# Kernel optimization log

Measured on AMD Instinct MI355X. Metric: run time of the kernel, lower is better.

Reference implementation:

```python
import jax, jax.numpy as jnp
import numpy as np

EMBED_DIM = 768
NUM_HEADS = 12
HEAD_DIM = EMBED_DIM // NUM_HEADS
B, N = 16, 512


def setup_inputs() -> dict:
    key = jax.random.key(0)
    ks = jax.random.split(key, 13)
    s = 1.0 / np.sqrt(EMBED_DIM)
    return {
        "query": jax.random.normal(ks[0], (B, N, EMBED_DIM), jnp.float32),
        "key_in": jax.random.normal(ks[1], (B, N, EMBED_DIM), jnp.float32),
        "value": jax.random.normal(ks[2], (B, N, EMBED_DIM), jnp.float32),
        "spatial_bias": jax.random.normal(ks[3], (B, N, N), jnp.float32),
        "edge_bias": jax.random.normal(ks[4], (B, N, N), jnp.float32),
        "Wq": jax.random.uniform(ks[5], (EMBED_DIM, EMBED_DIM), jnp.float32, -s, s),
        "bq": jax.random.uniform(ks[6], (EMBED_DIM,), jnp.float32, -s, s),
        "Wk": jax.random.uniform(ks[7], (EMBED_DIM, EMBED_DIM), jnp.float32, -s, s),
        "bk": jax.random.uniform(ks[8], (EMBED_DIM,), jnp.float32, -s, s),
        "Wv": jax.random.uniform(ks[9], (EMBED_DIM, EMBED_DIM), jnp.float32, -s, s),
        "bv": jax.random.uniform(ks[10], (EMBED_DIM,), jnp.float32, -s, s),
        "Wo": jax.random.uniform(ks[11], (EMBED_DIM, EMBED_DIM), jnp.float32, -s, s),
        "bo": jax.random.uniform(ks[12], (EMBED_DIM,), jnp.float32, -s, s),
    }


def reference(query, key_in, value, spatial_bias, edge_bias,
              Wq, bq, Wk, bk, Wv, bv, Wo, bo):
    b, n, e = query.shape
    h, d = NUM_HEADS, HEAD_DIM
    scale = d ** -0.5
    # projections (torch Linear: x @ W.T + b), reshape to [b, h, n, d]
    Q = (query @ Wq.T + bq).reshape(b, n, h, d).transpose(0, 2, 1, 3)
    K = (key_in @ Wk.T + bk).reshape(b, n, h, d).transpose(0, 2, 1, 3)
    V = (value @ Wv.T + bv).reshape(b, n, h, d).transpose(0, 2, 1, 3)
    # scores: [b, h, n, n] with additive spatial + edge bias broadcast over heads
    scores = jnp.einsum('bhnd,bhmd->bhnm', Q, K) * scale
    scores = scores + spatial_bias[:, None, :, :] + edge_bias[:, None, :, :]
    attn_weights = jax.nn.softmax(scores, axis=-1)
    attn_output = jnp.einsum('bhnm,bhmd->bhnd', attn_weights, V)
    attn_output = attn_output.transpose(0, 2, 1, 3).reshape(b, n, e)
    attn_output = attn_output @ Wo.T + bo
    return attn_output, attn_weights
```

## Files before the change

kernel.cpp:

```cpp
#include <hip/hip_runtime.h>

using bf16x8 = __attribute__((ext_vector_type(8))) __bf16;
using f32x4  = __attribute__((ext_vector_type(4))) float;
using u16 = unsigned short;

constexpr int Bb = 16, Nn = 512, Ee = 768, Hh = 12, Dd = 64;

__device__ inline u16 f2b(float x) {
  union { float f; unsigned int u; } v; v.f = x;
  unsigned int r = v.u + 0x7fffu + ((v.u >> 16) & 1u);
  return (u16)(r >> 16);
}

__device__ inline unsigned cvtpk(float lo, float hi) {
  unsigned r;
  asm("v_cvt_pk_bf16_f32 %0, %1, %2" : "=v"(r) : "v"(lo), "v"(hi));
  return r;
}

__device__ inline void gload16(const void* g, void* l) {
  __builtin_amdgcn_global_load_lds((const __attribute__((address_space(1))) void*)g,
                                   (__attribute__((address_space(3))) void*)l, 16, 0, 0);
}

#define MFMA __builtin_amdgcn_mfma_f32_16x16x32_bf16

__global__ void k_cvtw(const float* __restrict__ w0, const float* __restrict__ w1,
                       const float* __restrict__ w2, const float* __restrict__ w3,
                       u16* __restrict__ dst) {
  int idx = blockIdx.x * 256 + threadIdx.x;
  constexpr int per = Ee * Ee / 4;
  int m = idx / per, r = idx - m * per;
  const float* src = (m == 0) ? w0 : (m == 1) ? w1 : (m == 2) ? w2 : w3;
  float4 v = reinterpret_cast<const float4*>(src)[r];
  ushort4 o = make_ushort4(f2b(v.x), f2b(v.y), f2b(v.z), f2b(v.w));
  reinterpret_cast<ushort4*>(dst)[idx] = o;
}

__global__ void k_biascomb(const float* __restrict__ sb, const float* __restrict__ eb,
                           u16* __restrict__ cb) {
  int idx = blockIdx.x * 256 + threadIdx.x;
  float4 s0 = reinterpret_cast<const float4*>(sb)[idx * 2];
  float4 s1 = reinterpret_cast<const float4*>(sb)[idx * 2 + 1];
  float4 e0 = reinterpret_cast<const float4*>(eb)[idx * 2];
  float4 e1 = reinterpret_cast<const float4*>(eb)[idx * 2 + 1];
  ushort4 o0 = make_ushort4(f2b(s0.x + e0.x), f2b(s0.y + e0.y), f2b(s0.z + e0.z), f2b(s0.w + e0.w));
  ushort4 o1 = make_ushort4(f2b(s1.x + e1.x), f2b(s1.y + e1.y), f2b(s1.z + e1.z), f2b(s1.w + e1.w));
  reinterpret_cast<ushort4*>(cb)[idx * 2] = o0;
  reinterpret_cast<ushort4*>(cb)[idx * 2 + 1] = o1;
}

__global__ __launch_bounds__(256, 3)
void k_qkv(const float* __restrict__ xq, const float* __restrict__ xk, const float* __restrict__ xv,
           const u16* __restrict__ wb, const float* __restrict__ bq, const float* __restrict__ bk,
           const float* __restrict__ bv, u16* __restrict__ Q, u16* __restrict__ K,
           u16* __restrict__ VT) {
  const int mat = blockIdx.z;
  const float* X = (mat == 0) ? xq : (mat == 1) ? xk : xv;
  const u16* W = wb + (size_t)mat * Ee * Ee;
  const float* bias = (mat == 0) ? bq : (mat == 1) ? bk : bv;
  const int bm = blockIdx.x, bn = blockIdx.y;
  const int tid = threadIdx.x, lane = tid & 63, wid = tid >> 6;
  const int wr = wid >> 1, wc = wid & 1;

  __shared__ char smem[49152];

  auto stageA = [&](int buf, int it) {
    const int r0 = tid >> 3, s = tid & 7;
    char* lbase = smem + buf * 16384 + tid * 16;
#pragma unroll
    for (int R = 0; R < 4; ++R) {
      const int row = R * 32 + r0;
      const int ch = s ^ (row & 7);
      gload16(X + (size_t)(bm * 128 + row) * Ee + it * 32 + ch * 4, lbase + R * 4096);
    }
  };
  auto stageB = [&](int buf, int it) {
    const int r0 = tid >> 2, s = tid & 3;
    char* lbase = smem + 32768 + buf * 8192 + tid * 16;
#pragma unroll
    for (int R = 0; R < 2; ++R) {
      const int row = R * 64 + r0;
      const int ch = s ^ ((row >> 1) & 3);
      gload16(W + (size_t)(bn * 128 + row) * Ee + it * 32 + ch * 8, lbase + R * 4096);
    }
  };

  f32x4 acc[4][4] = {};

  auto compute = [&](int buf) {
    const char* Ab = smem + buf * 16384;
    const char* Bbp = smem + 32768 + buf * 8192;
    const int q = lane >> 4;
    bf16x8 a[4], b[4];
#pragma unroll
    for (int mt = 0; mt < 4; ++mt) {
      const int row = wr * 64 + mt * 16 + (lane & 15);
      const int s0 = (2 * q) ^ (row & 7), s1 = (2 * q + 1) ^ (row & 7);
      f32x4 f0 = *reinterpret_cast<const f32x4*>(Ab + row * 128 + s0 * 16);
      f32x4 f1 = *reinterpret_cast<const f32x4*>(Ab + row * 128 + s1 * 16);
      union { unsigned u[4]; bf16x8 v; } cv;
      cv.u[0] = cvtpk(f0[0], f0[1]);
      cv.u[1] = cvtpk(f0[2], f0[3]);
      cv.u[2] = cvtpk(f1[0], f1[1]);
      cv.u[3] = cvtpk(f1[2], f1[3]);
      a[mt] = cv.v;
    }
#pragma unroll
    for (int nt = 0; nt < 4; ++nt) {
      const int row = wc * 64 + nt * 16 + (lane & 15);
      const int s = q ^ ((row >> 1) & 3);
      b[nt] = *reinterpret_cast<const bf16x8*>(Bbp + row * 64 + s * 16);
    }
#pragma unroll
    for (int mt = 0; mt < 4; ++mt)
#pragma unroll
      for (int nt = 0; nt < 4; ++nt)
        acc[mt][nt] = MFMA(a[mt], b[nt], acc[mt][nt], 0, 0, 0);
  };

  stageA(0, 0); stageB(0, 0);
  __syncthreads();
  int buf = 0;
  for (int it = 0; it < 24; ++it) {
    if (it + 1 < 24) { stageA(buf ^ 1, it + 1); stageB(buf ^ 1, it + 1); }
    compute(buf);
    __syncthreads();
    buf ^= 1;
  }

  u16* sm16 = (u16*)smem;
  if (mat < 2) {
    u16* dst = (mat == 0) ? Q : K;
    const float sc = (mat == 0) ? 0.125f : 1.0f;
#pragma unroll
    for (int mt = 0; mt < 4; ++mt) {
      const int n_l0 = wr * 64 + mt * 16 + ((lane >> 4) << 2);
#pragma unroll
      for (int nt = 0; nt < 4; ++nt) {
        const int e_l = wc * 64 + nt * 16 + (lane & 15);
        const float bs = bias[bn * 128 + e_l];
#pragma unroll
        for (int j = 0; j < 4; ++j)
          sm16[(n_l0 + j) * 136 + e_l] = f2b((acc[mt][nt][j] + bs) * sc);
      }
    }
    __syncthreads();
    const int row = tid >> 1, half = tid & 1;
    const int n = bm * 128 + row, b = n >> 9, n0 = n & 511, h = bn * 2 + half;
    u16* gp = dst + ((size_t)(b * Hh + h) * Nn + n0) * Dd;
    const u16* sp = sm16 + row * 136 + half * 64;
#pragma unroll
    for (int i = 0; i < 8; ++i)
      *reinterpret_cast<int4*>(gp + i * 8) = *reinterpret_cast<const int4*>(sp + i * 8);
  } else {
#pragma unroll
    for (int mt = 0; mt < 4; ++mt) {
      const int n_l0 = wr * 64 + mt * 16 + ((lane >> 4) << 2);
#pragma unroll
      for (int nt = 0; nt < 4; ++nt) {
        const int e_l = wc * 64 + nt * 16 + (lane & 15);
        const float bs = bias[bn * 128 + e_l];
#pragma unroll
        for (int j = 0; j < 4; ++j)
          sm16[e_l * 136 + n_l0 + j] = f2b(acc[mt][nt][j] + bs);
      }
    }
    __syncthreads();
    const int er = tid >> 1, half = tid & 1;
    const int b = bm >> 2, h = bn * 2 + (er >> 6), d = er & 63;
    u16* gp = VT + ((size_t)(b * Hh + h) * Dd + d) * Nn + (bm & 3) * 128 + half * 64;
    const u16* sp = sm16 + er * 136 + half * 64;
#pragma unroll
    for (int i = 0; i < 8; ++i)
      *reinterpret_cast<int4*>(gp + i * 8) = *reinterpret_cast<const int4*>(sp + i * 8);
  }
}

__global__ __launch_bounds__(256, 2)
void k_attn(const u16* __restrict__ Q, const u16* __restrict__ K,
            const u16* __restrict__ cb, const u16* __restrict__ VT,
            float* __restrict__ wout, u16* __restrict__ AO) {
  const int qb = blockIdx.x, h = blockIdx.y, b = blockIdx.z;
  const int bh = b * Hh + h;
  const int q0 = qb * 64;
  const int tid = threadIdx.x, lane = tid & 63, wid = tid >> 6;
  const int l15 = lane & 15, q4 = lane >> 4;

  __shared__ char smem[65536];

  bf16x8 aq[2];
  {
    const u16* qp = Q + ((size_t)bh * Nn + q0 + wid * 16 + l15) * Dd + q4 * 8;
    aq[0] = *reinterpret_cast<const bf16x8*>(qp);
    aq[1] = *reinterpret_cast<const bf16x8*>(qp + 32);
  }

#pragma unroll
  for (int i = 0; i < 16; ++i) {
    const int s = i * 256 + tid;
    const int row = s >> 3, cs = s & 7;
    gload16(K + ((size_t)bh * Nn + row) * Dd + (cs ^ (row & 7)) * 8, smem + s * 16);
  }
  __syncthreads();

  f32x4 acc[32] = {};
#pragma unroll
  for (int kt = 0; kt < 8; ++kt)
#pragma unroll
    for (int kk = 0; kk < 2; ++kk)
#pragma unroll
      for (int ct = 0; ct < 4; ++ct) {
        const int r = kt * 64 + ct * 16 + l15;
        bf16x8 bk = *reinterpret_cast<const bf16x8*>(
            smem + r * 128 + (((kk * 4 + q4) ^ (r & 7)) * 16));
        acc[kt * 4 + ct] = MFMA(bk, aq[kk], acc[kt * 4 + ct], 0, 0, 0);
      }

  const int rql = wid * 16 + l15;
  const int rq = q0 + rql;
  const u16* cbp = cb + ((size_t)b * Nn + rq) * Nn + q4 * 4;
  uint2 cbr[32];
#pragma unroll
  for (int t = 0; t < 32; ++t)
    cbr[t] = *reinterpret_cast<const uint2*>(cbp + t * 16);
#pragma unroll
  for (int t = 0; t < 32; ++t) {
    acc[t][0] += __uint_as_float((unsigned)cbr[t].x << 16);
    acc[t][1] += __uint_as_float(cbr[t].x & 0xffff0000u);
    acc[t][2] += __uint_as_float((unsigned)cbr[t].y << 16);
    acc[t][3] += __uint_as_float(cbr[t].y & 0xffff0000u);
  }

  float mx = -1e30f;
#pragma unroll
  for (int t = 0; t < 32; ++t)
#pragma unroll
    for (int j = 0; j < 4; ++j) mx = fmaxf(mx, acc[t][j]);
  mx = fmaxf(mx, __shfl_xor(mx, 16));
  mx = fmaxf(mx, __shfl_xor(mx, 32));

  float sum = 0.f;
#pragma unroll
  for (int t = 0; t < 32; ++t)
#pragma unroll
    for (int j = 0; j < 4; ++j) {
      float p = exp2f((acc[t][j] - mx) * 1.44269504f);
      acc[t][j] = p;
      sum += p;
    }
  sum += __shfl_xor(sum, 16);
  sum += __shfl_xor(sum, 32);
  const float inv = 1.0f / sum;

  __syncthreads();

  const u16* Vb = VT + ((size_t)bh * Dd + l15) * Nn + q4 * 8;
  bf16x8 vb0[8], vb1[8];
  auto loadV = [&](int kt, bf16x8* d) {
#pragma unroll
    for (int kk = 0; kk < 2; ++kk)
#pragma unroll
      for (int ct = 0; ct < 4; ++ct)
        d[kk * 4 + ct] = *reinterpret_cast<const bf16x8*>(
            Vb + (size_t)(ct * 16) * Nn + kt * 64 + kk * 32);
  };
  loadV(0, vb0);
  loadV(1, vb1);

  f32x4* wp4 = reinterpret_cast<f32x4*>(wout + ((size_t)bh * Nn + rq) * Nn);
  char* Pb = smem + rql * 1024;
#pragma unroll
  for (int t = 0; t < 32; ++t) {
    f32x4 o;
    o[0] = acc[t][0] * inv; o[1] = acc[t][1] * inv;
    o[2] = acc[t][2] * inv; o[3] = acc[t][3] * inv;
    __builtin_nontemporal_store(o, &wp4[t * 4 + q4]);
    uint2 pk;
    pk.x = cvtpk(o[0], o[1]);
    pk.y = cvtpk(o[2], o[3]);
    const int chunk = (2 * t + (q4 >> 1)) ^ (rql & 7);
    *reinterpret_cast<uint2*>(Pb + chunk * 16 + (q4 & 1) * 8) = pk;
  }
  __syncthreads();

  f32x4 acc2[4] = {};
  const int qr = rql;
  const char* Pr = smem + qr * 1024;
#pragma unroll
  for (int kp = 0; kp < 4; ++kp) {
    const int ktA = 2 * kp, ktB = 2 * kp + 1;
#pragma unroll
    for (int kk = 0; kk < 2; ++kk) {
      const int chunk = (ktA * 8 + kk * 4 + q4) ^ (qr & 7);
      bf16x8 pa = *reinterpret_cast<const bf16x8*>(Pr + chunk * 16);
#pragma unroll
      for (int ct = 0; ct < 4; ++ct)
        acc2[ct] = MFMA(pa, vb0[kk * 4 + ct], acc2[ct], 0, 0, 0);
    }
    if (ktA + 2 < 8) loadV(ktA + 2, vb0);
#pragma unroll
    for (int kk = 0; kk < 2; ++kk) {
      const int chunk = (ktB * 8 + kk * 4 + q4) ^ (qr & 7);
      bf16x8 pa = *reinterpret_cast<const bf16x8*>(Pr + chunk * 16);
#pragma unroll
      for (int ct = 0; ct < 4; ++ct)
        acc2[ct] = MFMA(pa, vb1[kk * 4 + ct], acc2[ct], 0, 0, 0);
    }
    if (ktB + 2 < 8) loadV(ktB + 2, vb1);
  }

  __syncthreads();
  u16* ao_t = (u16*)smem;
#pragma unroll
  for (int ct = 0; ct < 4; ++ct)
#pragma unroll
    for (int j = 0; j < 4; ++j)
      ao_t[(wid * 16 + q4 * 4 + j) * 72 + ct * 16 + l15] = f2b(acc2[ct][j]);
  __syncthreads();
  {
    const int row = tid >> 3, ch = tid & 7;
#pragma unroll
    for (int i = 0; i < 2; ++i) {
      const int r = row + i * 32;
      int4 v = *reinterpret_cast<const int4*>(ao_t + r * 72 + ch * 8);
      *reinterpret_cast<int4*>(AO + ((size_t)b * Nn + q0 + r) * Ee + h * Dd + ch * 8) = v;
    }
  }
}

__global__ __launch_bounds__(256, 4)
void k_outproj(const u16* __restrict__ AOp, const u16* __restrict__ Wo,
               const float* __restrict__ bo, float* __restrict__ out) {
  const int bm = blockIdx.x, bn = blockIdx.y;
  const int tid = threadIdx.x, lane = tid & 63, wid = tid >> 6;
  const int wr = wid >> 1, wc = wid & 1;

  __shared__ char smem[32768];

  auto stage = [&](const u16* src, int lds_base, int buf, int it) {
    const int r0 = tid >> 2, s = tid & 3;
    char* lbase = smem + lds_base + buf * 8192 + tid * 16;
#pragma unroll
    for (int R = 0; R < 2; ++R) {
      const int row = R * 64 + r0;
      const int ch = s ^ ((row >> 1) & 3);
      gload16(src + (size_t)row * Ee + it * 32 + ch * 8, lbase + R * 4096);
    }
  };

  f32x4 acc[4][4] = {};

  auto compute = [&](int buf) {
    const char* Ab = smem + buf * 8192;
    const char* Bbp = smem + 16384 + buf * 8192;
    const int q = lane >> 4;
    bf16x8 a[4], b[4];
#pragma unroll
    for (int mt = 0; mt < 4; ++mt) {
      const int row = wr * 64 + mt * 16 + (lane & 15);
      const int s = q ^ ((row >> 1) & 3);
      a[mt] = *reinterpret_cast<const bf16x8*>(Ab + row * 64 + s * 16);
    }
#pragma unroll
    for (int nt = 0; nt < 4; ++nt) {
      const int row = wc * 64 + nt * 16 + (lane & 15);
      const int s = q ^ ((row >> 1) & 3);
      b[nt] = *reinterpret_cast<const bf16x8*>(Bbp + row * 64 + s * 16);
    }
#pragma unroll
    for (int mt = 0; mt < 4; ++mt)
#pragma unroll
      for (int nt = 0; nt < 4; ++nt)
        acc[mt][nt] = MFMA(a[mt], b[nt], acc[mt][nt], 0, 0, 0);
  };

  const u16* Asrc = AOp + (size_t)(bm * 128) * Ee;
  const u16* Bsrc = Wo + (size_t)(bn * 128) * Ee;
  stage(Asrc, 0, 0, 0); stage(Bsrc, 16384, 0, 0);
  __syncthreads();
  int buf = 0;
  for (int it = 0; it < 24; ++it) {
    if (it + 1 < 24) { stage(Asrc, 0, buf ^ 1, it + 1); stage(Bsrc, 16384, buf ^ 1, it + 1); }
    compute(buf);
    __syncthreads();
    buf ^= 1;
  }

#pragma unroll
  for (int mt = 0; mt < 4; ++mt) {
#pragma unroll
    for (int nt = 0; nt < 4; ++nt) {
      const int ecol = bn * 128 + wc * 64 + nt * 16 + (lane & 15);
      const int r0 = bm * 128 + wr * 64 + mt * 16 + ((lane >> 4) << 2);
      const float bs = bo[ecol];
      f32x4 v = acc[mt][nt];
#pragma unroll
      for (int j = 0; j < 4; ++j)
        out[(size_t)(r0 + j) * Ee + ecol] = v[j] + bs;
    }
  }
}

extern "C" void kernel_launch(void* const* d_in, const int* in_sizes, int n_in,
                              void* d_out, int out_size, void* d_ws, size_t ws_size,
                              hipStream_t stream) {
  const float* query  = (const float*)d_in[0];
  const float* key_in = (const float*)d_in[1];
  const float* value  = (const float*)d_in[2];
  const float* sb     = (const float*)d_in[3];
  const float* eb     = (const float*)d_in[4];
  const float* Wq     = (const float*)d_in[5];
  const float* bq     = (const float*)d_in[6];
  const float* Wk     = (const float*)d_in[7];
  const float* bk     = (const float*)d_in[8];
  const float* Wv     = (const float*)d_in[9];
  const float* bv     = (const float*)d_in[10];
  const float* Wo     = (const float*)d_in[11];
  const float* bo     = (const float*)d_in[12];

  float* out0 = (float*)d_out;
  float* wout = out0 + (size_t)Bb * Nn * Ee;

  char* ws = (char*)d_ws;
  const size_t off_wb = 0;
  const size_t off_Q  = 4718592;
  const size_t off_K  = 17301504;
  const size_t off_VT = 29884416;
  const size_t off_AO = 42467328;
  const size_t off_cb = 55050240;
  if (ws_size < 63438848) return;

  u16* wb  = (u16*)(ws + off_wb);
  u16* Qs  = (u16*)(ws + off_Q);
  u16* Kst = (u16*)(ws + off_K);
  u16* VTs = (u16*)(ws + off_VT);
  u16* AO  = (u16*)(ws + off_AO);
  u16* cbf = (u16*)(ws + off_cb);

  k_cvtw<<<2304, 256, 0, stream>>>(Wq, Wk, Wv, Wo, wb);
  k_biascomb<<<2048, 256, 0, stream>>>(sb, eb, cbf);
  k_qkv<<<dim3(64, 6, 3), 256, 0, stream>>>(query, key_in, value, wb, bq, bk, bv, Qs, Kst, VTs);
  k_attn<<<dim3(8, Hh, Bb), 256, 0, stream>>>(Qs, Kst, cbf, VTs, wout, AO);
  k_outproj<<<dim3(64, 6), 256, 0, stream>>>(AO, wb + 3 * Ee * Ee, bo, out0);
}
```

Before: 196.3 us.

## Fuse conversion kernels, remap attention blocks, overlap weight stores with PV MFMAs

Merges the weight-conversion and bias-combine kernels into a single launch to save a kernel launch. The attention kernel remaps its flat block index so that consecutive blocks cover different (batch, head) pairs at the same query tile. It also issues the combined-bias loads before the QK MFMAs to hide their latency and raises wave priority around the MFMA loops. The fp32 attention-weight stores are moved out of the P-packing loop and interleaved with the PV MFMA steps so the large write overlaps compute. The output-projection stores become nontemporal. Keeping acc live longer adds register pressure, which may hurt occupancy.

```diff
diff --git a/kernel.cpp b/kernel.cpp
--- a/kernel.cpp
+++ b/kernel.cpp
@@ -25,29 +25,31 @@
 
 #define MFMA __builtin_amdgcn_mfma_f32_16x16x32_bf16
 
-__global__ void k_cvtw(const float* __restrict__ w0, const float* __restrict__ w1,
-                       const float* __restrict__ w2, const float* __restrict__ w3,
-                       u16* __restrict__ dst) {
+__global__ void k_cvt(const float* __restrict__ w0, const float* __restrict__ w1,
+                      const float* __restrict__ w2, const float* __restrict__ w3,
+                      u16* __restrict__ dstW,
+                      const float* __restrict__ sb, const float* __restrict__ eb,
+                      u16* __restrict__ cb) {
   int idx = blockIdx.x * 256 + threadIdx.x;
-  constexpr int per = Ee * Ee / 4;
-  int m = idx / per, r = idx - m * per;
-  const float* src = (m == 0) ? w0 : (m == 1) ? w1 : (m == 2) ? w2 : w3;
-  float4 v = reinterpret_cast<const float4*>(src)[r];
-  ushort4 o = make_ushort4(f2b(v.x), f2b(v.y), f2b(v.z), f2b(v.w));
-  reinterpret_cast<ushort4*>(dst)[idx] = o;
-}
-
-__global__ void k_biascomb(const float* __restrict__ sb, const float* __restrict__ eb,
-                           u16* __restrict__ cb) {
-  int idx = blockIdx.x * 256 + threadIdx.x;
-  float4 s0 = reinterpret_cast<const float4*>(sb)[idx * 2];
-  float4 s1 = reinterpret_cast<const float4*>(sb)[idx * 2 + 1];
-  float4 e0 = reinterpret_cast<const float4*>(eb)[idx * 2];
-  float4 e1 = reinterpret_cast<const float4*>(eb)[idx * 2 + 1];
-  ushort4 o0 = make_ushort4(f2b(s0.x + e0.x), f2b(s0.y + e0.y), f2b(s0.z + e0.z), f2b(s0.w + e0.w));
-  ushort4 o1 = make_ushort4(f2b(s1.x + e1.x), f2b(s1.y + e1.y), f2b(s1.z + e1.z), f2b(s1.w + e1.w));
-  reinterpret_cast<ushort4*>(cb)[idx * 2] = o0;
-  reinterpret_cast<ushort4*>(cb)[idx * 2 + 1] = o1;
+  constexpr int perW = Ee * Ee / 4;
+  constexpr int totW = 4 * perW;
+  if (idx < totW) {
+    int m = idx / perW, r = idx - m * perW;
+    const float* src = (m == 0) ? w0 : (m == 1) ? w1 : (m == 2) ? w2 : w3;
+    float4 v = reinterpret_cast<const float4*>(src)[r];
+    ushort4 o = make_ushort4(f2b(v.x), f2b(v.y), f2b(v.z), f2b(v.w));
+    reinterpret_cast<ushort4*>(dstW)[idx] = o;
+  } else {
+    int k = idx - totW;
+    float4 s0 = reinterpret_cast<const float4*>(sb)[k * 2];
+    float4 s1 = reinterpret_cast<const float4*>(sb)[k * 2 + 1];
+    float4 e0 = reinterpret_cast<const float4*>(eb)[k * 2];
+    float4 e1 = reinterpret_cast<const float4*>(eb)[k * 2 + 1];
+    ushort4 o0 = make_ushort4(f2b(s0.x + e0.x), f2b(s0.y + e0.y), f2b(s0.z + e0.z), f2b(s0.w + e0.w));
+    ushort4 o1 = make_ushort4(f2b(s1.x + e1.x), f2b(s1.y + e1.y), f2b(s1.z + e1.z), f2b(s1.w + e1.w));
+    reinterpret_cast<ushort4*>(cb)[k * 2] = o0;
+    reinterpret_cast<ushort4*>(cb)[k * 2 + 1] = o1;
+  }
 }
 
 __global__ __launch_bounds__(256, 3)
@@ -181,7 +183,11 @@
 void k_attn(const u16* __restrict__ Q, const u16* __restrict__ K,
             const u16* __restrict__ cb, const u16* __restrict__ VT,
             float* __restrict__ wout, u16* __restrict__ AO) {
-  const int qb = blockIdx.x, h = blockIdx.y, b = blockIdx.z;
+  const int flat = blockIdx.x + 8 * (blockIdx.y + Hh * blockIdx.z);
+  const int c = flat & 7, j = flat >> 3;
+  const int g = c + 8 * (j % 24);
+  const int qb = j / 24;
+  const int h = g % Hh, b = g / Hh;
   const int bh = b * Hh + h;
   const int q0 = qb * 64;
   const int tid = threadIdx.x, lane = tid & 63, wid = tid >> 6;
@@ -196,6 +202,14 @@
     aq[1] = *reinterpret_cast<const bf16x8*>(qp + 32);
   }
 
+  const int rql = wid * 16 + l15;
+  const int rq = q0 + rql;
+  const u16* cbp = cb + ((size_t)b * Nn + rq) * Nn + q4 * 4;
+  uint2 cbr[32];
+#pragma unroll
+  for (int t = 0; t < 32; ++t)
+    cbr[t] = *reinterpret_cast<const uint2*>(cbp + t * 16);
+
 #pragma unroll
   for (int i = 0; i < 16; ++i) {
     const int s = i * 256 + tid;
@@ -205,6 +219,7 @@
   __syncthreads();
 
   f32x4 acc[32] = {};
+  __builtin_amdgcn_s_setprio(1);
 #pragma unroll
   for (int kt = 0; kt < 8; ++kt)
 #pragma unroll
@@ -216,14 +231,8 @@
             smem + r * 128 + (((kk * 4 + q4) ^ (r & 7)) * 16));
         acc[kt * 4 + ct] = MFMA(bk, aq[kk], acc[kt * 4 + ct], 0, 0, 0);
       }
-
-  const int rql = wid * 16 + l15;
-  const int rq = q0 + rql;
-  const u16* cbp = cb + ((size_t)b * Nn + rq) * Nn + q4 * 4;
-  uint2 cbr[32];
-#pragma unroll
-  for (int t = 0; t < 32; ++t)
-    cbr[t] = *reinterpret_cast<const uint2*>(cbp + t * 16);
+  __builtin_amdgcn_s_setprio(0);
+
 #pragma unroll
   for (int t = 0; t < 32; ++t) {
     acc[t][0] += __uint_as_float((unsigned)cbr[t].x << 16);
@@ -236,7 +245,7 @@
 #pragma unroll
   for (int t = 0; t < 32; ++t)
 #pragma unroll
-    for (int j = 0; j < 4; ++j) mx = fmaxf(mx, acc[t][j]);
+    for (int j2 = 0; j2 < 4; ++j2) mx = fmaxf(mx, acc[t][j2]);
   mx = fmaxf(mx, __shfl_xor(mx, 16));
   mx = fmaxf(mx, __shfl_xor(mx, 32));
 
@@ -244,9 +253,9 @@
 #pragma unroll
   for (int t = 0; t < 32; ++t)
 #pragma unroll
-    for (int j = 0; j < 4; ++j) {
-      float p = exp2f((acc[t][j] - mx) * 1.44269504f);
-      acc[t][j] = p;
+    for (int j2 = 0; j2 < 4; ++j2) {
+      float p = exp2f((acc[t][j2] - mx) * 1.44269504f);
+      acc[t][j2] = p;
       sum += p;
     }
   sum += __shfl_xor(sum, 16);
@@ -268,17 +277,12 @@
   loadV(0, vb0);
   loadV(1, vb1);
 
-  f32x4* wp4 = reinterpret_cast<f32x4*>(wout + ((size_t)bh * Nn + rq) * Nn);
   char* Pb = smem + rql * 1024;
 #pragma unroll
   for (int t = 0; t < 32; ++t) {
-    f32x4 o;
-    o[0] = acc[t][0] * inv; o[1] = acc[t][1] * inv;
-    o[2] = acc[t][2] * inv; o[3] = acc[t][3] * inv;
-    __builtin_nontemporal_store(o, &wp4[t * 4 + q4]);
     uint2 pk;
-    pk.x = cvtpk(o[0], o[1]);
-    pk.y = cvtpk(o[2], o[3]);
+    pk.x = cvtpk(acc[t][0] * inv, acc[t][1] * inv);
+    pk.y = cvtpk(acc[t][2] * inv, acc[t][3] * inv);
     const int chunk = (2 * t + (q4 >> 1)) ^ (rql & 7);
     *reinterpret_cast<uint2*>(Pb + chunk * 16 + (q4 & 1) * 8) = pk;
   }
@@ -287,9 +291,21 @@
   f32x4 acc2[4] = {};
   const int qr = rql;
   const char* Pr = smem + qr * 1024;
+  f32x4* wp4 = reinterpret_cast<f32x4*>(wout + ((size_t)bh * Nn + rq) * Nn);
+  auto storeW = [&](int kt) {
+#pragma unroll
+    for (int u = 0; u < 4; ++u) {
+      const int t = kt * 4 + u;
+      f32x4 o;
+      o[0] = acc[t][0] * inv; o[1] = acc[t][1] * inv;
+      o[2] = acc[t][2] * inv; o[3] = acc[t][3] * inv;
+      __builtin_nontemporal_store(o, &wp4[t * 4 + q4]);
+    }
+  };
 #pragma unroll
   for (int kp = 0; kp < 4; ++kp) {
     const int ktA = 2 * kp, ktB = 2 * kp + 1;
+    __builtin_amdgcn_s_setprio(1);
 #pragma unroll
     for (int kk = 0; kk < 2; ++kk) {
       const int chunk = (ktA * 8 + kk * 4 + q4) ^ (qr & 7);
@@ -298,7 +314,10 @@
       for (int ct = 0; ct < 4; ++ct)
         acc2[ct] = MFMA(pa, vb0[kk * 4 + ct], acc2[ct], 0, 0, 0);
     }
+    __builtin_amdgcn_s_setprio(0);
     if (ktA + 2 < 8) loadV(ktA + 2, vb0);
+    storeW(ktA);
+    __builtin_amdgcn_s_setprio(1);
 #pragma unroll
     for (int kk = 0; kk < 2; ++kk) {
       const int chunk = (ktB * 8 + kk * 4 + q4) ^ (qr & 7);
@@ -307,7 +326,9 @@
       for (int ct = 0; ct < 4; ++ct)
         acc2[ct] = MFMA(pa, vb1[kk * 4 + ct], acc2[ct], 0, 0, 0);
     }
+    __builtin_amdgcn_s_setprio(0);
     if (ktB + 2 < 8) loadV(ktB + 2, vb1);
+    storeW(ktB);
   }
 
   __syncthreads();
@@ -315,8 +336,8 @@
 #pragma unroll
   for (int ct = 0; ct < 4; ++ct)
 #pragma unroll
-    for (int j = 0; j < 4; ++j)
-      ao_t[(wid * 16 + q4 * 4 + j) * 72 + ct * 16 + l15] = f2b(acc2[ct][j]);
+    for (int j2 = 0; j2 < 4; ++j2)
+      ao_t[(wid * 16 + q4 * 4 + j2) * 72 + ct * 16 + l15] = f2b(acc2[ct][j2]);
   __syncthreads();
   {
     const int row = tid >> 3, ch = tid & 7;
@@ -397,7 +418,7 @@
       f32x4 v = acc[mt][nt];
 #pragma unroll
       for (int j = 0; j < 4; ++j)
-        out[(size_t)(r0 + j) * Ee + ecol] = v[j] + bs;
+        __builtin_nontemporal_store(v[j] + bs, &out[(size_t)(r0 + j) * Ee + ecol]);
     }
   }
 }
@@ -438,8 +459,7 @@
   u16* AO  = (u16*)(ws + off_AO);
   u16* cbf = (u16*)(ws + off_cb);
 
-  k_cvtw<<<2304, 256, 0, stream>>>(Wq, Wk, Wv, Wo, wb);
-  k_biascomb<<<2048, 256, 0, stream>>>(sb, eb, cbf);
+  k_cvt<<<4352, 256, 0, stream>>>(Wq, Wk, Wv, Wo, wb, sb, eb, cbf);
   k_qkv<<<dim3(64, 6, 3), 256, 0, stream>>>(query, key_in, value, wb, bq, bk, bv, Qs, Kst, VTs);
   k_attn<<<dim3(8, Hh, Bb), 256, 0, stream>>>(Qs, Kst, cbf, VTs, wout, AO);
   k_outproj<<<dim3(64, 6), 256, 0, stream>>>(AO, wb + 3 * Ee * Ee, bo, out0);
```

After: 175.3 us. 1.12x faster.
